# Kernel tuning notes

Measured on AMD Instinct MI355X. Metric: run time of the kernel, lower is better.

Reference implementation:

```python
import jax, jax.numpy as jnp
import numpy as np

# FP4 (e2m1) representable magnitudes: {0, 0.5, 1, 1.5, 2, 3, 4, 6}
_FP4_GRID = np.array([0.0, 0.5, 1.0, 1.5, 2.0, 3.0, 4.0, 6.0], dtype=np.float32)
_FP4_MIDS = (_FP4_GRID[1:] + _FP4_GRID[:-1]) / 2.0  # decision boundaries


def quant_fp4(x):
    """Per-tensor symmetric quantize-dequantize to FP4 e2m1 grid."""
    grid = jnp.asarray(_FP4_GRID, dtype=x.dtype)
    mids = jnp.asarray(_FP4_MIDS, dtype=x.dtype)
    scale = jnp.maximum(jnp.max(jnp.abs(x)) / 6.0, jnp.asarray(1e-12, x.dtype))
    xs = jnp.abs(x) / scale
    idx = jnp.searchsorted(mids, xs)  # nearest-grid-point index
    return jnp.sign(x) * grid[idx] * scale


def fp4_linear(x, w, b):
    # fake-quantized matmul: dequant(FP4(x)) @ dequant(FP4(w)) + b
    return jnp.matmul(quant_fp4(x), quant_fp4(w)) + b


def setup_inputs() -> dict:
    key = jax.random.key(0)
    k1, k2, k3 = jax.random.split(key, 3)
    B, D_IN, D_H, D_OUT = 4096, 4096, 16384, 4096
    x = jax.random.normal(k1, (B, D_IN), dtype=jnp.float32)
    w1 = jax.random.normal(k2, (D_IN, D_H), dtype=jnp.float32)
    b1 = jnp.zeros((D_H,), dtype=jnp.float32)
    w2 = jax.random.normal(k3, (D_H, D_OUT), dtype=jnp.float32)
    b2 = jnp.zeros((D_OUT,), dtype=jnp.float32)
    return {"x": x, "w1": w1, "b1": b1, "w2": w2, "b2": b2}


def reference(x, w1, b1, w2, b2):
    h = jax.nn.relu(fp4_linear(x, w1, b1))
    return fp4_linear(h, w2, b2)
```

## Files before the change

### kernel.cpp

```cpp
#include <hip/hip_runtime.h>
#include <hip/hip_bf16.h>


typedef float f32x4 __attribute__((ext_vector_type(4)));
typedef int   i32x4 __attribute__((ext_vector_type(4)));
typedef int   i32x8 __attribute__((ext_vector_type(8)));

#define AS1 __attribute__((address_space(1)))
#define AS3 __attribute__((address_space(3)))

__device__ __forceinline__ float scale_from_amax_bits(unsigned bits) {
    return fmaxf(__uint_as_float(bits) / 6.0f, 1e-12f);
}

__device__ __forceinline__ unsigned q4(float v, float inv_scale) {
    float xs = fabsf(v) * inv_scale;
    unsigned idx = 0;
    idx += (xs > 0.25f);
    idx += (xs > 0.75f);
    idx += (xs > 1.25f);
    idx += (xs > 1.75f);
    idx += (xs > 2.5f);
    idx += (xs > 3.5f);
    idx += (xs > 5.0f);
    return idx | ((v < 0.0f) ? 8u : 0u);
}

__global__ void zero4_kernel(unsigned* p) {
    if (threadIdx.x < 4) p[threadIdx.x] = 0u;
}

__global__ void sentinel_kernel(float* out, long long n) {
    long long i = (long long)blockIdx.x * blockDim.x + threadIdx.x;
    long long stride = (long long)gridDim.x * blockDim.x;
    for (; i < n; i += stride) out[i] = 1e30f;
}

__global__ void absmax_kernel(const float* __restrict__ in, long long n,
                              unsigned* __restrict__ out) {
    long long i = ((long long)blockIdx.x * blockDim.x + threadIdx.x) * 4;
    long long stride = (long long)gridDim.x * blockDim.x * 4;
    float m = 0.0f;
    for (; i < n; i += stride) {
        float4 v = *(const float4*)&in[i];
        m = fmaxf(m, fmaxf(fmaxf(fabsf(v.x), fabsf(v.y)),
                           fmaxf(fabsf(v.z), fabsf(v.w))));
    }
    #pragma unroll
    for (int off = 32; off > 0; off >>= 1)
        m = fmaxf(m, __shfl_xor(m, off));
    __shared__ float smax[4];
    int lane = threadIdx.x & 63, w = threadIdx.x >> 6;
    if (lane == 0) smax[w] = m;
    __syncthreads();
    if (threadIdx.x == 0) {
        m = fmaxf(fmaxf(smax[0], smax[1]), fmaxf(smax[2], smax[3]));
        atomicMax(out, __float_as_uint(m));
    }
}

__global__ void quant_pack_kernel(const float* __restrict__ in, long long n,
                                  const unsigned* __restrict__ amax,
                                  unsigned* __restrict__ out) {
    float inv = 1.0f / scale_from_amax_bits(*amax);
    long long i = ((long long)blockIdx.x * blockDim.x + threadIdx.x) * 8;
    long long stride = (long long)gridDim.x * blockDim.x * 8;
    for (; i < n; i += stride) {
        float4 a = *(const float4*)&in[i];
        float4 b = *(const float4*)&in[i + 4];
        unsigned u = q4(a.x, inv)        | (q4(a.y, inv) << 4)
                   | (q4(a.z, inv) << 8) | (q4(a.w, inv) << 12)
                   | (q4(b.x, inv) << 16)| (q4(b.y, inv) << 20)
                   | (q4(b.z, inv) << 24)| (q4(b.w, inv) << 28);
        out[i >> 3] = u;
    }
}

__global__ void quant_transpose_pack_kernel(const float* __restrict__ in, int R, int C,
                                            const unsigned* __restrict__ amax,
                                            unsigned char* __restrict__ out) {
    __shared__ float tile[64][65];
    float inv = 1.0f / scale_from_amax_bits(*amax);
    int t = threadIdx.x;
    int CT = C >> 6;
    int tc = blockIdx.x % CT;
    int tr = blockIdx.x / CT;
    int r0 = t >> 4;
    int c0 = (t & 15) * 4;
    #pragma unroll
    for (int it = 0; it < 4; ++it) {
        int r = r0 + it * 16;
        float4 v = *(const float4*)&in[(size_t)(tr * 64 + r) * C + tc * 64 + c0];
        tile[r][c0 + 0] = v.x;
        tile[r][c0 + 1] = v.y;
        tile[r][c0 + 2] = v.z;
        tile[r][c0 + 3] = v.w;
    }
    __syncthreads();
    int c = t >> 2;
    int rch = (t & 3) * 16;
    unsigned u0 = 0, u1 = 0;
    #pragma unroll
    for (int j = 0; j < 8; ++j) u0 |= q4(tile[rch + j][c], inv) << (4 * j);
    #pragma unroll
    for (int j = 0; j < 8; ++j) u1 |= q4(tile[rch + 8 + j][c], inv) << (4 * j);
    uint2 o; o.x = u0; o.y = u1;
    *(uint2*)&out[(size_t)(tc * 64 + c) * (R >> 1) + (size_t)(tr * 32) + (rch >> 1)] = o;
}

template <int RELU, int FUSE_AMAX>
__global__ __launch_bounds__(256, 2)
void gemm_fp4_kernel(const unsigned char* __restrict__ Ap,
                     const unsigned char* __restrict__ Bp,
                     float* __restrict__ C, const float* __restrict__ bias,
                     const unsigned* __restrict__ amaxA,
                     const unsigned* __restrict__ amaxB,
                     unsigned* __restrict__ amaxOut,
                     int M, int N, int K) {
    __shared__ alignas(16) unsigned char As[128 * 128];
    __shared__ alignas(16) unsigned char Bs[128 * 128];
    __shared__ float smax[4];

    int nwg = gridDim.x;
    int cpx = nwg >> 3;
    int wg = (blockIdx.x & 7) * cpx + (blockIdx.x >> 3);
    int MT = M >> 7;
    int tm = wg % MT;
    int tn = wg / MT;

    int tid = threadIdx.x;
    int lane = tid & 63;
    int wid = tid >> 6;
    int wr = wid >> 1, wc = wid & 1;

    size_t Kb = (size_t)(K >> 1);

    int cs = ((lane & 7) ^ ((lane >> 3) & 7)) << 4;
    int srow = wid * 32 + (lane >> 3);
    const unsigned char* Abase = Ap + (size_t)(tm * 128 + srow) * Kb + cs;
    const unsigned char* Bbase = Bp + (size_t)(tn * 128 + srow) * Kb + cs;
    char* AsB = (char*)As;
    char* BsB = (char*)Bs;
    int ldsOff = wid * 4096;

    f32x4 acc[4][4] = {};

    int rrA = wr * 64 + (lane & 15);
    int rrB = wc * 64 + (lane & 15);

    int KT = K >> 8;
    for (int kt = 0; kt < KT; ++kt) {
        #pragma unroll
        for (int i = 0; i < 4; ++i) {
            __builtin_amdgcn_global_load_lds(
                (const AS1 void*)(Abase + (size_t)kt * 128 + (size_t)(i * 8) * Kb),
                (AS3 void*)(AsB + ldsOff + i * 1024), 16, 0, 0);
            __builtin_amdgcn_global_load_lds(
                (const AS1 void*)(Bbase + (size_t)kt * 128 + (size_t)(i * 8) * Kb),
                (AS3 void*)(BsB + ldsOff + i * 1024), 16, 0, 0);
        }
        __syncthreads();

        #pragma unroll
        for (int ks = 0; ks < 2; ++ks) {
            int slotOff = ((ks * 4 + (lane >> 4)) ^ (lane & 7)) << 4;
            i32x8 a8[4], b8[4];
            #pragma unroll
            for (int mi = 0; mi < 4; ++mi) {
                i32x4 v = *(const i32x4*)(AsB + (rrA + mi * 16) * 128 + slotOff);
                a8[mi] = i32x8{v[0], v[1], v[2], v[3], 0, 0, 0, 0};
            }
            #pragma unroll
            for (int ni = 0; ni < 4; ++ni) {
                i32x4 v = *(const i32x4*)(BsB + (rrB + ni * 16) * 128 + slotOff);
                b8[ni] = i32x8{v[0], v[1], v[2], v[3], 0, 0, 0, 0};
            }
            #pragma unroll
            for (int mi = 0; mi < 4; ++mi)
                #pragma unroll
                for (int ni = 0; ni < 4; ++ni)
                    acc[mi][ni] = __builtin_amdgcn_mfma_scale_f32_16x16x128_f8f6f4(
                        a8[mi], b8[ni], acc[mi][ni],
                        4, 4,
                        0, 0x7f7f7f7f,
                        0, 0x7f7f7f7f);
        }
        __syncthreads();
    }

    float sa = scale_from_amax_bits(*amaxA);
    float sb = scale_from_amax_bits(*amaxB);
    float s = sa * sb;
    float vmax = 0.0f;
    int rowBase = tm * 128 + wr * 64 + (lane >> 4) * 4;
    int colBase = tn * 128 + wc * 64 + (lane & 15);
    #pragma unroll
    for (int mi = 0; mi < 4; ++mi) {
        #pragma unroll
        for (int ni = 0; ni < 4; ++ni) {
            int col = colBase + ni * 16;
            float bv = bias[col];
            int row = rowBase + mi * 16;
            #pragma unroll
            for (int r = 0; r < 4; ++r) {
                float v = acc[mi][ni][r] * s + bv;
                if (RELU) v = fmaxf(v, 0.0f);
                if (FUSE_AMAX) vmax = fmaxf(vmax, fabsf(v));
                C[(size_t)(row + r) * N + col] = v;
            }
        }
    }
    if (FUSE_AMAX) {
        #pragma unroll
        for (int off = 32; off > 0; off >>= 1)
            vmax = fmaxf(vmax, __shfl_xor(vmax, off));
        if (lane == 0) smax[wid] = vmax;
        __syncthreads();
        if (tid == 0) {
            vmax = fmaxf(fmaxf(smax[0], smax[1]), fmaxf(smax[2], smax[3]));
            atomicMax(amaxOut, __float_as_uint(vmax));
        }
    }
}

extern "C" void kernel_launch(void* const* d_in, const int* in_sizes, int n_in,
                              void* d_out, int out_size, void* d_ws, size_t ws_size,
                              hipStream_t stream) {
    const float* x  = (const float*)d_in[0];
    const float* w1 = (const float*)d_in[1];
    const float* b1 = (const float*)d_in[2];
    const float* w2 = (const float*)d_in[3];
    const float* b2 = (const float*)d_in[4];
    float* out = (float*)d_out;

    const int B = 4096, DIN = 4096, DH = 16384, DOUT = 4096;

    const size_t off_amax = 0;
    const size_t off_Xq   = 256;
    const size_t off_W    = off_Xq + (size_t)B * DIN / 2;
    const size_t off_h    = off_W + (size_t)DIN * DH / 2;
    const size_t off_Hq   = off_h + (size_t)B * DH * 4;
    const size_t needed   = off_Hq + (size_t)B * DH / 2;

    if (ws_size < needed) {
        sentinel_kernel<<<2048, 256, 0, stream>>>(out, (long long)out_size);
        return;
    }

    char* ws = (char*)d_ws;
    unsigned* amax = (unsigned*)(ws + off_amax);
    unsigned char* Xq = (unsigned char*)(ws + off_Xq);
    unsigned char* Wq = (unsigned char*)(ws + off_W);
    float*         h  = (float*)(ws + off_h);
    unsigned char* Hq = (unsigned char*)(ws + off_Hq);

    zero4_kernel<<<1, 64, 0, stream>>>(amax);

    absmax_kernel<<<2048, 256, 0, stream>>>(x, (long long)B * DIN, amax + 0);
    absmax_kernel<<<2048, 256, 0, stream>>>(w1, (long long)DIN * DH, amax + 1);
    absmax_kernel<<<2048, 256, 0, stream>>>(w2, (long long)DH * DOUT, amax + 3);

    quant_pack_kernel<<<2048, 256, 0, stream>>>(x, (long long)B * DIN, amax + 0,
                                                (unsigned*)Xq);
    quant_transpose_pack_kernel<<<(DIN / 64) * (DH / 64), 256, 0, stream>>>(
        w1, DIN, DH, amax + 1, Wq);

    gemm_fp4_kernel<1, 1><<<(B / 128) * (DH / 128), 256, 0, stream>>>(
        Xq, Wq, h, b1, amax + 0, amax + 1, amax + 2, B, DH, DIN);

    quant_pack_kernel<<<2048, 256, 0, stream>>>(h, (long long)B * DH, amax + 2,
                                                (unsigned*)Hq);
    quant_transpose_pack_kernel<<<(DH / 64) * (DOUT / 64), 256, 0, stream>>>(
        w2, DH, DOUT, amax + 3, Wq);

    gemm_fp4_kernel<0, 0><<<(B / 128) * (DOUT / 128), 256, 0, stream>>>(
        Hq, Wq, out, b2, amax + 2, amax + 3, nullptr, B, DOUT, DH);
}
```

Before: 691.2 us.

## Rewrite FP4 GEMM as 256x256 double-buffered 8-wave pipeline with 32x32 MFMA

Replaces the 128x128, 4-wave, single-buffered FP4 GEMM with a 256x256 tile, 8-wave kernel that double-buffers LDS and interleaves global-to-LDS prefetch of the next K-slice with four MFMA phases per iteration. It switches from 16x16x128 to 32x32x64 scaled MFMA, raises wave priority during MFMA bursts, and uses raw barriers with explicit vmcnt waits. The aim is to hide global-load latency and improve data reuse per byte loaded. In exchange it uses 128KB of LDS per block, which limits occupancy, and it relies on carefully hand-ordered synchronisation.

After: 742.4 us, median of 4. 1.07x slower.

```diff
diff --git a/kernel.cpp b/kernel.cpp
--- a/kernel.cpp
+++ b/kernel.cpp
@@ -2,12 +2,18 @@
 #include <hip/hip_bf16.h>
 
 
-typedef float f32x4 __attribute__((ext_vector_type(4)));
-typedef int   i32x4 __attribute__((ext_vector_type(4)));
-typedef int   i32x8 __attribute__((ext_vector_type(8)));
+typedef float f32x16 __attribute__((ext_vector_type(16)));
+typedef int   i32x4  __attribute__((ext_vector_type(4)));
+typedef int   i32x8  __attribute__((ext_vector_type(8)));
 
 #define AS1 __attribute__((address_space(1)))
 #define AS3 __attribute__((address_space(3)))
+
+__device__ __forceinline__ void wg_barrier() {
+    asm volatile("" ::: "memory");
+    __builtin_amdgcn_s_barrier();
+    asm volatile("" ::: "memory");
+}
 
 __device__ __forceinline__ float scale_from_amax_bits(unsigned bits) {
     return fmaxf(__uint_as_float(bits) / 6.0f, 1e-12f);
@@ -108,105 +114,181 @@
     *(uint2*)&out[(size_t)(tc * 64 + c) * (R >> 1) + (size_t)(tr * 32) + (rch >> 1)] = o;
 }
 
+__device__ __forceinline__ f32x16 mm_fp4(i32x4 a, i32x4 b, f32x16 c) {
+    i32x8 a8 = {a[0], a[1], a[2], a[3], 0, 0, 0, 0};
+    i32x8 b8 = {b[0], b[1], b[2], b[3], 0, 0, 0, 0};
+    return __builtin_amdgcn_mfma_scale_f32_32x32x64_f8f6f4(
+        a8, b8, c, 4, 4,
+        0, 0x7f7f7f7f,
+        0, 0x7f7f7f7f);
+}
+
 template <int RELU, int FUSE_AMAX>
-__global__ __launch_bounds__(256, 2)
-void gemm_fp4_kernel(const unsigned char* __restrict__ Ap,
-                     const unsigned char* __restrict__ Bp,
-                     float* __restrict__ C, const float* __restrict__ bias,
-                     const unsigned* __restrict__ amaxA,
-                     const unsigned* __restrict__ amaxB,
-                     unsigned* __restrict__ amaxOut,
-                     int M, int N, int K) {
-    __shared__ alignas(16) unsigned char As[128 * 128];
-    __shared__ alignas(16) unsigned char Bs[128 * 128];
-    __shared__ float smax[4];
+__global__ __launch_bounds__(512, 2)
+void gemm_fp4_8ph(const unsigned char* __restrict__ Ap,
+                  const unsigned char* __restrict__ Bp,
+                  float* __restrict__ C, const float* __restrict__ bias,
+                  const unsigned* __restrict__ amaxA,
+                  const unsigned* __restrict__ amaxB,
+                  unsigned* __restrict__ amaxOut,
+                  int M, int N, int K) {
+    __shared__ alignas(16) unsigned char As[65536];
+    __shared__ alignas(16) unsigned char Bs[65536];
+    __shared__ float smax[8];
 
     int nwg = gridDim.x;
     int cpx = nwg >> 3;
     int wg = (blockIdx.x & 7) * cpx + (blockIdx.x >> 3);
-    int MT = M >> 7;
+    int MT = M >> 8;
     int tm = wg % MT;
     int tn = wg / MT;
 
     int tid = threadIdx.x;
     int lane = tid & 63;
     int wid = tid >> 6;
-    int wr = wid >> 1, wc = wid & 1;
+    int wr = wid >> 2;
+    int wc = wid & 3;
 
     size_t Kb = (size_t)(K >> 1);
 
-    int cs = ((lane & 7) ^ ((lane >> 3) & 7)) << 4;
-    int srow = wid * 32 + (lane >> 3);
-    const unsigned char* Abase = Ap + (size_t)(tm * 128 + srow) * Kb + cs;
-    const unsigned char* Bbase = Bp + (size_t)(tn * 128 + srow) * Kb + cs;
+    int srow = tid >> 3;
+    int scs = ((tid & 7) ^ (srow & 7)) << 4;
+    const unsigned char* Ag = Ap + ((size_t)(tm * 256) + srow) * Kb + scs;
+    const unsigned char* Bg = Bp + ((size_t)(tn * 256) + srow) * Kb + scs;
     char* AsB = (char*)As;
     char* BsB = (char*)Bs;
-    int ldsOff = wid * 4096;
-
-    f32x4 acc[4][4] = {};
-
-    int rrA = wr * 64 + (lane & 15);
-    int rrB = wc * 64 + (lane & 15);
+    int stageOff = wid << 10;
+
+#define STG_A(d, h, j, kt)                                                     \
+    __builtin_amdgcn_global_load_lds(                                          \
+        (const AS1 void*)(Ag + (size_t)((h) * 128 + (j) * 64) * Kb +           \
+                          (size_t)(kt) * 128),                                 \
+        (AS3 void*)(AsB + ((d) << 15) + ((h) << 14) + ((j) << 13) + stageOff), \
+        16, 0, 0)
+#define STG_B(d, h, j, kt)                                                     \
+    __builtin_amdgcn_global_load_lds(                                          \
+        (const AS1 void*)(Bg + (size_t)((h) * 128 + (j) * 64) * Kb +           \
+                          (size_t)(kt) * 128),                                 \
+        (AS3 void*)(BsB + ((d) << 15) + ((h) << 14) + ((j) << 13) + stageOff), \
+        16, 0, 0)
+#define STG_AH(d, h, kt) do { STG_A(d, h, 0, kt); STG_A(d, h, 1, kt); } while (0)
+#define STG_BH(d, h, kt) do { STG_B(d, h, 0, kt); STG_B(d, h, 1, kt); } while (0)
+
+    int l31 = lane & 31, l7 = lane & 7, kh = lane >> 5;
+    const char* Ard = AsB + (wr << 14) + l31 * 128;
+    const char* Brd = BsB + ((wc >> 1) << 14) + ((wc & 1) << 13) + l31 * 128;
+    int so[4];
+    #pragma unroll
+    for (int ks = 0; ks < 4; ++ks) so[ks] = (((ks * 2 + kh) ^ l7) << 4);
+
+    f32x16 acc[4][2] = {};
 
     int KT = K >> 8;
-    for (int kt = 0; kt < KT; ++kt) {
-        #pragma unroll
-        for (int i = 0; i < 4; ++i) {
-            __builtin_amdgcn_global_load_lds(
-                (const AS1 void*)(Abase + (size_t)kt * 128 + (size_t)(i * 8) * Kb),
-                (AS3 void*)(AsB + ldsOff + i * 1024), 16, 0, 0);
-            __builtin_amdgcn_global_load_lds(
-                (const AS1 void*)(Bbase + (size_t)kt * 128 + (size_t)(i * 8) * Kb),
-                (AS3 void*)(BsB + ldsOff + i * 1024), 16, 0, 0);
-        }
-        __syncthreads();
-
-        #pragma unroll
-        for (int ks = 0; ks < 2; ++ks) {
-            int slotOff = ((ks * 4 + (lane >> 4)) ^ (lane & 7)) << 4;
-            i32x8 a8[4], b8[4];
-            #pragma unroll
-            for (int mi = 0; mi < 4; ++mi) {
-                i32x4 v = *(const i32x4*)(AsB + (rrA + mi * 16) * 128 + slotOff);
-                a8[mi] = i32x8{v[0], v[1], v[2], v[3], 0, 0, 0, 0};
-            }
-            #pragma unroll
-            for (int ni = 0; ni < 4; ++ni) {
-                i32x4 v = *(const i32x4*)(BsB + (rrB + ni * 16) * 128 + slotOff);
-                b8[ni] = i32x8{v[0], v[1], v[2], v[3], 0, 0, 0, 0};
-            }
-            #pragma unroll
-            for (int mi = 0; mi < 4; ++mi)
+
+    STG_AH(0, 0, 0); STG_AH(0, 1, 0);
+    STG_BH(0, 0, 0); STG_BH(0, 1, 0);
+    STG_AH(1, 0, 1);
+    asm volatile("s_waitcnt vmcnt(2)" ::: "memory");
+    wg_barrier();
+
+    for (int t = 0; t < KT; ++t) {
+        int d = t & 1, dn = d ^ 1;
+        int dOff = d << 15;
+        const char* Aq = Ard + dOff;
+        const char* Bq = Brd + dOff;
+        i32x4 a0[2][4], a1[2][4], b0[4], b1[4];
+
+        #pragma unroll
+        for (int mi = 0; mi < 2; ++mi)
+            #pragma unroll
+            for (int ks = 0; ks < 4; ++ks)
+                a0[mi][ks] = *(const i32x4*)(Aq + mi * 4096 + so[ks]);
+        #pragma unroll
+        for (int ks = 0; ks < 4; ++ks)
+            b0[ks] = *(const i32x4*)(Bq + so[ks]);
+        if (t + 1 < KT) STG_AH(dn, 1, t + 1);
+        wg_barrier();
+        __builtin_amdgcn_s_setprio(1);
+        __builtin_amdgcn_sched_barrier(0);
+        #pragma unroll
+        for (int mi = 0; mi < 2; ++mi)
+            #pragma unroll
+            for (int ks = 0; ks < 4; ++ks)
+                acc[mi][0] = mm_fp4(a0[mi][ks], b0[ks], acc[mi][0]);
+        __builtin_amdgcn_sched_barrier(0);
+        __builtin_amdgcn_s_setprio(0);
+        wg_barrier();
+
+        #pragma unroll
+        for (int ks = 0; ks < 4; ++ks)
+            b1[ks] = *(const i32x4*)(Bq + 4096 + so[ks]);
+        if (t + 1 < KT) STG_BH(dn, 0, t + 1);
+        wg_barrier();
+        __builtin_amdgcn_s_setprio(1);
+        __builtin_amdgcn_sched_barrier(0);
+        #pragma unroll
+        for (int mi = 0; mi < 2; ++mi)
+            #pragma unroll
+            for (int ks = 0; ks < 4; ++ks)
+                acc[mi][1] = mm_fp4(a0[mi][ks], b1[ks], acc[mi][1]);
+        __builtin_amdgcn_sched_barrier(0);
+        __builtin_amdgcn_s_setprio(0);
+        wg_barrier();
+
+        #pragma unroll
+        for (int mi = 0; mi < 2; ++mi)
+            #pragma unroll
+            for (int ks = 0; ks < 4; ++ks)
+                a1[mi][ks] = *(const i32x4*)(Aq + (2 + mi) * 4096 + so[ks]);
+        if (t + 1 < KT) STG_BH(dn, 1, t + 1);
+        wg_barrier();
+        __builtin_amdgcn_s_setprio(1);
+        __builtin_amdgcn_sched_barrier(0);
+        #pragma unroll
+        for (int mi = 0; mi < 2; ++mi)
+            #pragma unroll
+            for (int ks = 0; ks < 4; ++ks)
+                acc[2 + mi][1] = mm_fp4(a1[mi][ks], b1[ks], acc[2 + mi][1]);
+        __builtin_amdgcn_sched_barrier(0);
+        __builtin_amdgcn_s_setprio(0);
+        wg_barrier();
+
+        if (t + 2 < KT) STG_AH(d, 0, t + 2);
+        wg_barrier();
+        __builtin_amdgcn_s_setprio(1);
+        __builtin_amdgcn_sched_barrier(0);
+        #pragma unroll
+        for (int mi = 0; mi < 2; ++mi)
+            #pragma unroll
+            for (int ks = 0; ks < 4; ++ks)
+                acc[2 + mi][0] = mm_fp4(a1[mi][ks], b0[ks], acc[2 + mi][0]);
+        __builtin_amdgcn_sched_barrier(0);
+        __builtin_amdgcn_s_setprio(0);
+        if (t + 2 < KT) { asm volatile("s_waitcnt vmcnt(2)" ::: "memory"); }
+        else            { asm volatile("s_waitcnt vmcnt(0)" ::: "memory"); }
+        wg_barrier();
+        (void)dn;
+    }
+
+    float s = scale_from_amax_bits(*amaxA) * scale_from_amax_bits(*amaxB);
+    float vmax = 0.0f;
+    int colBase = tn * 256 + wc * 64 + l31;
+    int rowB0 = tm * 256 + wr * 128 + (kh << 2);
+    #pragma unroll
+    for (int mi = 0; mi < 4; ++mi) {
+        #pragma unroll
+        for (int ni = 0; ni < 2; ++ni) {
+            int col = colBase + ni * 32;
+            float bv = bias[col];
+            #pragma unroll
+            for (int rg = 0; rg < 4; ++rg) {
                 #pragma unroll
-                for (int ni = 0; ni < 4; ++ni)
-                    acc[mi][ni] = __builtin_amdgcn_mfma_scale_f32_16x16x128_f8f6f4(
-                        a8[mi], b8[ni], acc[mi][ni],
-                        4, 4,
-                        0, 0x7f7f7f7f,
-                        0, 0x7f7f7f7f);
-        }
-        __syncthreads();
-    }
-
-    float sa = scale_from_amax_bits(*amaxA);
-    float sb = scale_from_amax_bits(*amaxB);
-    float s = sa * sb;
-    float vmax = 0.0f;
-    int rowBase = tm * 128 + wr * 64 + (lane >> 4) * 4;
-    int colBase = tn * 128 + wc * 64 + (lane & 15);
-    #pragma unroll
-    for (int mi = 0; mi < 4; ++mi) {
-        #pragma unroll
-        for (int ni = 0; ni < 4; ++ni) {
-            int col = colBase + ni * 16;
-            float bv = bias[col];
-            int row = rowBase + mi * 16;
-            #pragma unroll
-            for (int r = 0; r < 4; ++r) {
-                float v = acc[mi][ni][r] * s + bv;
-                if (RELU) v = fmaxf(v, 0.0f);
-                if (FUSE_AMAX) vmax = fmaxf(vmax, fabsf(v));
-                C[(size_t)(row + r) * N + col] = v;
+                for (int rr = 0; rr < 4; ++rr) {
+                    float v = acc[mi][ni][rg * 4 + rr] * s + bv;
+                    if (RELU) v = fmaxf(v, 0.0f);
+                    if (FUSE_AMAX) vmax = fmaxf(vmax, fabsf(v));
+                    C[(size_t)(rowB0 + mi * 32 + rg * 8 + rr) * N + col] = v;
+                }
             }
         }
     }
@@ -217,10 +299,16 @@
         if (lane == 0) smax[wid] = vmax;
         __syncthreads();
         if (tid == 0) {
-            vmax = fmaxf(fmaxf(smax[0], smax[1]), fmaxf(smax[2], smax[3]));
-            atomicMax(amaxOut, __float_as_uint(vmax));
+            float m = smax[0];
+            #pragma unroll
+            for (int i = 1; i < 8; ++i) m = fmaxf(m, smax[i]);
+            atomicMax(amaxOut, __float_as_uint(m));
         }
     }
+#undef STG_A
+#undef STG_B
+#undef STG_AH
+#undef STG_BH
 }
 
 extern "C" void kernel_launch(void* const* d_in, const int* in_sizes, int n_in,
@@ -265,7 +353,7 @@
     quant_transpose_pack_kernel<<<(DIN / 64) * (DH / 64), 256, 0, stream>>>(
         w1, DIN, DH, amax + 1, Wq);
 
-    gemm_fp4_kernel<1, 1><<<(B / 128) * (DH / 128), 256, 0, stream>>>(
+    gemm_fp4_8ph<1, 1><<<(B / 256) * (DH / 256), 512, 0, stream>>>(
         Xq, Wq, h, b1, amax + 0, amax + 1, amax + 2, B, DH, DIN);
 
     quant_pack_kernel<<<2048, 256, 0, stream>>>(h, (long long)B * DH, amax + 2,
@@ -273,6 +361,6 @@
     quant_transpose_pack_kernel<<<(DH / 64) * (DOUT / 64), 256, 0, stream>>>(
         w2, DH, DOUT, amax + 3, Wq);
 
-    gemm_fp4_kernel<0, 0><<<(B / 128) * (DOUT / 128), 256, 0, stream>>>(
+    gemm_fp4_8ph<0, 0><<<(B / 256) * (DOUT / 256), 512, 0, stream>>>(
         Hq, Wq, out, b2, amax + 2, amax + 3, nullptr, B, DOUT, DH);
 }
```

## Double-buffer FP4 GEMM LDS tiles and merge three absmax launches

Applied to the files above, without the earlier changes.

The GEMM now keeps two LDS stages for the A and B tiles and issues the global-to-LDS loads for the next K tile before computing on the current one, so load latency can overlap with MFMA work. The three absmax reductions are merged into one launch that splits its blocks across x, w1 and w2, which removes launch gaps. LDS use per block doubles to 64KB, which may cut occupancy below the two blocks per CU requested by the launch bounds. The loop keeps only one barrier per iteration, placed after compute. No wait on the prefetch (vmcnt) is visible before the next iteration reads that buffer, so there is a possible ordering race.

After: 753.6 us. 9.0% more time.

```diff
diff --git a/kernel.cpp b/kernel.cpp
--- a/kernel.cpp
+++ b/kernel.cpp
@@ -36,10 +36,20 @@
     for (; i < n; i += stride) out[i] = 1e30f;
 }
 
-__global__ void absmax_kernel(const float* __restrict__ in, long long n,
-                              unsigned* __restrict__ out) {
-    long long i = ((long long)blockIdx.x * blockDim.x + threadIdx.x) * 4;
-    long long stride = (long long)gridDim.x * blockDim.x * 4;
+__global__ void absmax3_kernel(const float* __restrict__ in0, long long n0,
+                               const float* __restrict__ in1, long long n1,
+                               const float* __restrict__ in2, long long n2,
+                               unsigned* __restrict__ out) {
+    const float* in;
+    long long n;
+    unsigned* o;
+    long long nb, b = blockIdx.x;
+    if (b < 512)       { in = in0; n = n0; o = out + 0; b -= 0;    nb = 512;  }
+    else if (b < 2560) { in = in1; n = n1; o = out + 1; b -= 512;  nb = 2048; }
+    else               { in = in2; n = n2; o = out + 3; b -= 2560; nb = 2048; }
+
+    long long i = (b * blockDim.x + threadIdx.x) * 4;
+    long long stride = nb * blockDim.x * 4;
     float m = 0.0f;
     for (; i < n; i += stride) {
         float4 v = *(const float4*)&in[i];
@@ -55,7 +65,7 @@
     __syncthreads();
     if (threadIdx.x == 0) {
         m = fmaxf(fmaxf(smax[0], smax[1]), fmaxf(smax[2], smax[3]));
-        atomicMax(out, __float_as_uint(m));
+        atomicMax(o, __float_as_uint(m));
     }
 }
 
@@ -110,15 +120,15 @@
 
 template <int RELU, int FUSE_AMAX>
 __global__ __launch_bounds__(256, 2)
-void gemm_fp4_kernel(const unsigned char* __restrict__ Ap,
-                     const unsigned char* __restrict__ Bp,
-                     float* __restrict__ C, const float* __restrict__ bias,
-                     const unsigned* __restrict__ amaxA,
-                     const unsigned* __restrict__ amaxB,
-                     unsigned* __restrict__ amaxOut,
-                     int M, int N, int K) {
-    __shared__ alignas(16) unsigned char As[128 * 128];
-    __shared__ alignas(16) unsigned char Bs[128 * 128];
+void gemm_fp4_dbuf(const unsigned char* __restrict__ Ap,
+                   const unsigned char* __restrict__ Bp,
+                   float* __restrict__ C, const float* __restrict__ bias,
+                   const unsigned* __restrict__ amaxA,
+                   const unsigned* __restrict__ amaxB,
+                   unsigned* __restrict__ amaxOut,
+                   int M, int N, int K) {
+    __shared__ alignas(16) unsigned char As[2][128 * 128];
+    __shared__ alignas(16) unsigned char Bs[2][128 * 128];
     __shared__ float smax[4];
 
     int nwg = gridDim.x;
@@ -143,36 +153,51 @@
     char* BsB = (char*)Bs;
     int ldsOff = wid * 4096;
 
+#define STAGE(d, kt)                                                          \
+    do {                                                                      \
+        _Pragma("unroll")                                                     \
+        for (int i_ = 0; i_ < 4; ++i_) {                                      \
+            __builtin_amdgcn_global_load_lds(                                 \
+                (const AS1 void*)(Abase + (size_t)(kt) * 128 +                \
+                                  (size_t)(i_ * 8) * Kb),                     \
+                (AS3 void*)(AsB + ((d) << 14) + ldsOff + i_ * 1024),          \
+                16, 0, 0);                                                    \
+            __builtin_amdgcn_global_load_lds(                                 \
+                (const AS1 void*)(Bbase + (size_t)(kt) * 128 +                \
+                                  (size_t)(i_ * 8) * Kb),                     \
+                (AS3 void*)(BsB + ((d) << 14) + ldsOff + i_ * 1024),          \
+                16, 0, 0);                                                    \
+        }                                                                     \
+    } while (0)
+
     f32x4 acc[4][4] = {};
-
     int rrA = wr * 64 + (lane & 15);
     int rrB = wc * 64 + (lane & 15);
 
     int KT = K >> 8;
-    for (int kt = 0; kt < KT; ++kt) {
-        #pragma unroll
-        for (int i = 0; i < 4; ++i) {
-            __builtin_amdgcn_global_load_lds(
-                (const AS1 void*)(Abase + (size_t)kt * 128 + (size_t)(i * 8) * Kb),
-                (AS3 void*)(AsB + ldsOff + i * 1024), 16, 0, 0);
-            __builtin_amdgcn_global_load_lds(
-                (const AS1 void*)(Bbase + (size_t)kt * 128 + (size_t)(i * 8) * Kb),
-                (AS3 void*)(BsB + ldsOff + i * 1024), 16, 0, 0);
-        }
-        __syncthreads();
-
+
+    STAGE(0, 0);
+    __syncthreads();
+
+    for (int t = 0; t < KT; ++t) {
+        int d = t & 1;
+        if (t + 1 < KT) STAGE(d ^ 1, t + 1);
+        __builtin_amdgcn_sched_barrier(0);
+
+        const char* Aq = AsB + (d << 14);
+        const char* Bq = BsB + (d << 14);
         #pragma unroll
         for (int ks = 0; ks < 2; ++ks) {
             int slotOff = ((ks * 4 + (lane >> 4)) ^ (lane & 7)) << 4;
             i32x8 a8[4], b8[4];
             #pragma unroll
             for (int mi = 0; mi < 4; ++mi) {
-                i32x4 v = *(const i32x4*)(AsB + (rrA + mi * 16) * 128 + slotOff);
+                i32x4 v = *(const i32x4*)(Aq + (rrA + mi * 16) * 128 + slotOff);
                 a8[mi] = i32x8{v[0], v[1], v[2], v[3], 0, 0, 0, 0};
             }
             #pragma unroll
             for (int ni = 0; ni < 4; ++ni) {
-                i32x4 v = *(const i32x4*)(BsB + (rrB + ni * 16) * 128 + slotOff);
+                i32x4 v = *(const i32x4*)(Bq + (rrB + ni * 16) * 128 + slotOff);
                 b8[ni] = i32x8{v[0], v[1], v[2], v[3], 0, 0, 0, 0};
             }
             #pragma unroll
@@ -187,6 +212,7 @@
         }
         __syncthreads();
     }
+#undef STAGE
 
     float sa = scale_from_amax_bits(*amaxA);
     float sb = scale_from_amax_bits(*amaxB);
@@ -256,16 +282,16 @@
 
     zero4_kernel<<<1, 64, 0, stream>>>(amax);
 
-    absmax_kernel<<<2048, 256, 0, stream>>>(x, (long long)B * DIN, amax + 0);
-    absmax_kernel<<<2048, 256, 0, stream>>>(w1, (long long)DIN * DH, amax + 1);
-    absmax_kernel<<<2048, 256, 0, stream>>>(w2, (long long)DH * DOUT, amax + 3);
+    absmax3_kernel<<<4608, 256, 0, stream>>>(x, (long long)B * DIN,
+                                             w1, (long long)DIN * DH,
+                                             w2, (long long)DH * DOUT, amax);
 
     quant_pack_kernel<<<2048, 256, 0, stream>>>(x, (long long)B * DIN, amax + 0,
                                                 (unsigned*)Xq);
     quant_transpose_pack_kernel<<<(DIN / 64) * (DH / 64), 256, 0, stream>>>(
         w1, DIN, DH, amax + 1, Wq);
 
-    gemm_fp4_kernel<1, 1><<<(B / 128) * (DH / 128), 256, 0, stream>>>(
+    gemm_fp4_dbuf<1, 1><<<(B / 128) * (DH / 128), 256, 0, stream>>>(
         Xq, Wq, h, b1, amax + 0, amax + 1, amax + 2, B, DH, DIN);
 
     quant_pack_kernel<<<2048, 256, 0, stream>>>(h, (long long)B * DH, amax + 2,
@@ -273,6 +299,6 @@
     quant_transpose_pack_kernel<<<(DH / 64) * (DOUT / 64), 256, 0, stream>>>(
         w2, DH, DOUT, amax + 3, Wq);
 
-    gemm_fp4_kernel<0, 0><<<(B / 128) * (DOUT / 128), 256, 0, stream>>>(
+    gemm_fp4_dbuf<0, 0><<<(B / 128) * (DOUT / 128), 256, 0, stream>>>(
         Hq, Wq, out, b2, amax + 2, amax + 3, nullptr, B, DOUT, DH);
 }
```
